# Kernel tuning notes

Hardware: AMD Instinct MI355X
Metric: run time of the kernel (lower is better)

Reference implementation:

```python
import jax, jax.numpy as jnp
import numpy as np
from jax import lax

K = 8  # diffusion channels
T = 3  # diffusion steps


def setup_inputs() -> dict:
    key = jax.random.key(0)
    k1, k2, k3 = jax.random.split(key, 3)
    x = jax.random.normal(k1, (16, 1, 512, 512), dtype=jnp.float32)
    # per-step conv weights [T, out=k, in=1, kh, kw] and biases [T, k]
    W = jax.random.normal(k2, (T, K, 1, 3, 3), dtype=jnp.float32) * 0.1
    b = jax.random.normal(k3, (T, K), dtype=jnp.float32) * 0.1
    return {"x": x, "W": W, "b": b}


def _g(d):
    # mode 1 edge-stopping function: exp(-|d| / (1 + d^2))
    return jnp.exp(-jnp.abs(d) / (1.0 + d * d))


def reference(x, W, b):
    in_x = x  # [N,1,H,W]
    for t in range(T):
        d1 = lax.conv_general_dilated(
            in_x, W[t], window_strides=(1, 1), padding="SAME",
            dimension_numbers=("NCHW", "OIHW", "NCHW"),
        ) + b[t][None, :, None, None]  # [N,K,H,W]
        features = _g(d1) * d1
        # squash_tensor: sum over the K channels, keep channel dim of 1
        in_x = in_x - jnp.sum(features, axis=1, keepdims=True) / K
    return in_x
```

## Files before the change

### kernel.cpp

```cpp
#include <hip/hip_runtime.h>

static constexpr int IMG = 512;
static constexpr int TX  = 64;
static constexpr int TY  = 16;
static constexpr int LST = 72;
static constexpr int SROWS  = TY + 6;
static constexpr int NSTAGE = SROWS * 18;

template<int WOFF, int NR, int RLO, int NG, bool TO_GLOBAL>
__device__ __forceinline__ void diffuse_step(
    const float* __restrict__ prev, float* __restrict__ cur,
    const float* __restrict__ Wt, const float* __restrict__ bt,
    int xoff, int ty0, int tx0, int tid, float* __restrict__ gout)
{
    constexpr int LOADW  = WOFF ? 8 : 6;
    constexpr int NITEMS = NR * NG;

    float L0[LOADW], L1[LOADW], L2[LOADW];
    {
        const int idx0 = (tid < NITEMS) ? tid : 0;
        const int rr = idx0 / NG, j = idx0 - rr * NG;
        const float* base = prev + (RLO + rr - 1) * LST + 4 * j;
        *(float4*)&L0[0] = *(const float4*)(base);
        *(float4*)&L1[0] = *(const float4*)(base + LST);
        *(float4*)&L2[0] = *(const float4*)(base + 2 * LST);
        if (WOFF) {
            *(float4*)&L0[4] = *(const float4*)(base + 4);
            *(float4*)&L1[4] = *(const float4*)(base + LST + 4);
            *(float4*)&L2[4] = *(const float4*)(base + 2 * LST + 4);
        } else {
            *(float2*)&L0[4] = *(const float2*)(base + 4);
            *(float2*)&L1[4] = *(const float2*)(base + LST + 4);
            *(float2*)&L2[4] = *(const float2*)(base + 2 * LST + 4);
        }
    }

    for (int idx = tid; idx < NITEMS; idx += 64) {
        float P0[LOADW], P1[LOADW], P2[LOADW];
        {
            const int nidx = (idx + 64 < NITEMS) ? (idx + 64) : idx;
            const int rr = nidx / NG, j = nidx - rr * NG;
            const float* base = prev + (RLO + rr - 1) * LST + 4 * j;
            *(float4*)&P0[0] = *(const float4*)(base);
            *(float4*)&P1[0] = *(const float4*)(base + LST);
            *(float4*)&P2[0] = *(const float4*)(base + 2 * LST);
            if (WOFF) {
                *(float4*)&P0[4] = *(const float4*)(base + 4);
                *(float4*)&P1[4] = *(const float4*)(base + LST + 4);
                *(float4*)&P2[4] = *(const float4*)(base + 2 * LST + 4);
            } else {
                *(float2*)&P0[4] = *(const float2*)(base + 4);
                *(float2*)&P1[4] = *(const float2*)(base + LST + 4);
                *(float2*)&P2[4] = *(const float2*)(base + 2 * LST + 4);
            }
        }

        const int rr = idx / NG, j = idx - rr * NG;
        const int r  = RLO + rr, c0 = 4 * j;

        float acc[4] = {0.f, 0.f, 0.f, 0.f};
#pragma unroll
        for (int k = 0; k < 8; ++k) {
            const float w0 = Wt[9*k+0], w1 = Wt[9*k+1], w2 = Wt[9*k+2];
            const float w3 = Wt[9*k+3], w4 = Wt[9*k+4], w5 = Wt[9*k+5];
            const float w6 = Wt[9*k+6], w7 = Wt[9*k+7], w8 = Wt[9*k+8];
            const float bk = bt[k];
#pragma unroll
            for (int i = 0; i < 4; ++i) {
                float d = bk;
                d = fmaf(w0, L0[WOFF+i],   d);
                d = fmaf(w1, L0[WOFF+i+1], d);
                d = fmaf(w2, L0[WOFF+i+2], d);
                d = fmaf(w3, L1[WOFF+i],   d);
                d = fmaf(w4, L1[WOFF+i+1], d);
                d = fmaf(w5, L1[WOFF+i+2], d);
                d = fmaf(w6, L2[WOFF+i],   d);
                d = fmaf(w7, L2[WOFF+i+1], d);
                d = fmaf(w8, L2[WOFF+i+2], d);
                const float t    = fmaf(d, d, 1.0f);
                const float rinv = __builtin_amdgcn_rcpf(t);
                const float e    = __builtin_amdgcn_exp2f(
                                       -1.442695040888963f * __builtin_fabsf(d) * rinv);
                acc[i] = fmaf(e, d, acc[i]);
            }
        }

        float4 v;
        v.x = L1[WOFF+1] - acc[0] * 0.125f;
        v.y = L1[WOFF+2] - acc[1] * 0.125f;
        v.z = L1[WOFF+3] - acc[2] * 0.125f;
        v.w = L1[WOFF+4] - acc[3] * 0.125f;

        const int gy = ty0 - 3 + r;
        if (TO_GLOBAL) {
            *(float4*)&gout[gy * IMG + tx0 + c0] = v;
        } else {
            const bool ry  = (unsigned)gy < (unsigned)IMG;
            const int  gx0 = xoff + c0;
            v.x = (ry && (unsigned)(gx0 + 0) < (unsigned)IMG) ? v.x : 0.f;
            v.y = (ry && (unsigned)(gx0 + 1) < (unsigned)IMG) ? v.y : 0.f;
            v.z = (ry && (unsigned)(gx0 + 2) < (unsigned)IMG) ? v.z : 0.f;
            v.w = (ry && (unsigned)(gx0 + 3) < (unsigned)IMG) ? v.w : 0.f;
            *(float4*)&cur[r * LST + c0] = v;
        }

#pragma unroll
        for (int q = 0; q < LOADW; ++q) { L0[q] = P0[q]; L1[q] = P1[q]; L2[q] = P2[q]; }
    }
}

__global__ __launch_bounds__(64) void deep_ad_kernel(
    const float* __restrict__ x, const float* __restrict__ W,
    const float* __restrict__ b, float* __restrict__ out)
{
    __shared__ float A[SROWS * LST];
    __shared__ float Bs[SROWS * LST];

    const int tid = threadIdx.x;
    const int tx0 = blockIdx.x * TX;
    const int ty0 = blockIdx.y * TY;
    const float* xin  = x   + (size_t)blockIdx.z * (IMG * IMG);
    float*       gout = out + (size_t)blockIdx.z * (IMG * IMG);

    {
        float4 sv[7];
#pragma unroll
        for (int q = 0; q < 7; ++q) {
            const int item = tid + 64 * q;
            const int rr = item / 18, j = item - rr * 18;
            const int gy = ty0 - 3 + rr;
            const int gx = tx0 - 4 + 4 * j;
            float4 v = {0.f, 0.f, 0.f, 0.f};
            if (item < NSTAGE && (unsigned)gy < (unsigned)IMG && (unsigned)gx < (unsigned)IMG)
                v = *(const float4*)(xin + gy * IMG + gx);
            sv[q] = v;
        }
#pragma unroll
        for (int q = 0; q < 7; ++q) {
            const int item = tid + 64 * q;
            if (item < NSTAGE) *(float4*)&A[item * 4] = sv[q];
        }
    }
    __syncthreads();

    diffuse_step<1, TY + 4, 1, 17, false>(A,  Bs, W + 0,   b + 0,  tx0 - 2, ty0, tx0, tid, nullptr);
    __syncthreads();
    diffuse_step<0, TY + 2, 2, 17, false>(Bs, A,  W + 72,  b + 8,  tx0 - 1, ty0, tx0, tid, nullptr);
    __syncthreads();
    diffuse_step<0, TY,     3, 16, true >(A, nullptr, W + 144, b + 16, 0, ty0, tx0, tid, gout);
}

extern "C" void kernel_launch(void* const* d_in, const int* in_sizes, int n_in,
                              void* d_out, int out_size, void* d_ws, size_t ws_size,
                              hipStream_t stream)
{
    const float* x = (const float*)d_in[0];
    const float* W = (const float*)d_in[1];
    const float* b = (const float*)d_in[2];
    float* out = (float*)d_out;
    const int N = in_sizes[0] / (IMG * IMG);
    dim3 grid(IMG / TX, IMG / TY, N);
    deep_ad_kernel<<<grid, 64, 0, stream>>>(x, W, b, out);
}
```

Measured before the change: 126.7 us.

## Double tile height and block size, fully unroll per-thread work loop

Tile height goes from 16 to 32 rows and the block from 64 to 128 threads. This cuts the fraction of halo rows recomputed across the three fused diffusion steps (recompute overhead drops from about 10/16 toward 10/32 of rows). The work loop becomes a compile-time unrolled trip count with clamped indices and guarded stores, so the last trip runs partially idle. Shared memory per block roughly doubles and the grid has half as many blocks, which may reduce occupancy and tail balance.

```diff
diff --git a/kernel.cpp b/kernel.cpp
--- a/kernel.cpp
+++ b/kernel.cpp
@@ -2,7 +2,8 @@
 
 static constexpr int IMG = 512;
 static constexpr int TX  = 64;
-static constexpr int TY  = 16;
+static constexpr int TY  = 32;
+static constexpr int NT  = 128;
 static constexpr int LST = 72;
 static constexpr int SROWS  = TY + 6;
 static constexpr int NSTAGE = SROWS * 18;
@@ -15,11 +16,12 @@
 {
     constexpr int LOADW  = WOFF ? 8 : 6;
     constexpr int NITEMS = NR * NG;
+    constexpr int TRIPS  = (NITEMS + NT - 1) / NT;
 
     float L0[LOADW], L1[LOADW], L2[LOADW];
     {
-        const int idx0 = (tid < NITEMS) ? tid : 0;
-        const int rr = idx0 / NG, j = idx0 - rr * NG;
+        const int cidx = (tid < NITEMS) ? tid : (NITEMS - 1);
+        const int rr = cidx / NG, j = cidx - rr * NG;
         const float* base = prev + (RLO + rr - 1) * LST + 4 * j;
         *(float4*)&L0[0] = *(const float4*)(base);
         *(float4*)&L1[0] = *(const float4*)(base + LST);
@@ -35,10 +37,14 @@
         }
     }
 
-    for (int idx = tid; idx < NITEMS; idx += 64) {
+#pragma unroll
+    for (int q = 0; q < TRIPS; ++q) {
+        const int idx = tid + q * NT;
+
         float P0[LOADW], P1[LOADW], P2[LOADW];
-        {
-            const int nidx = (idx + 64 < NITEMS) ? (idx + 64) : idx;
+        if (q + 1 < TRIPS) {
+            const int nidx = (tid + (q + 1) * NT < NITEMS) ? (tid + (q + 1) * NT)
+                                                           : (NITEMS - 1);
             const int rr = nidx / NG, j = nidx - rr * NG;
             const float* base = prev + (RLO + rr - 1) * LST + 4 * j;
             *(float4*)&P0[0] = *(const float4*)(base);
@@ -55,7 +61,8 @@
             }
         }
 
-        const int rr = idx / NG, j = idx - rr * NG;
+        const int cidx = (idx < NITEMS) ? idx : (NITEMS - 1);
+        const int rr = cidx / NG, j = cidx - rr * NG;
         const int r  = RLO + rr, c0 = 4 * j;
 
         float acc[4] = {0.f, 0.f, 0.f, 0.f};
@@ -93,7 +100,8 @@
 
         const int gy = ty0 - 3 + r;
         if (TO_GLOBAL) {
-            *(float4*)&gout[gy * IMG + tx0 + c0] = v;
+            if (idx < NITEMS)
+                *(float4*)&gout[gy * IMG + tx0 + c0] = v;
         } else {
             const bool ry  = (unsigned)gy < (unsigned)IMG;
             const int  gx0 = xoff + c0;
@@ -101,15 +109,16 @@
             v.y = (ry && (unsigned)(gx0 + 1) < (unsigned)IMG) ? v.y : 0.f;
             v.z = (ry && (unsigned)(gx0 + 2) < (unsigned)IMG) ? v.z : 0.f;
             v.w = (ry && (unsigned)(gx0 + 3) < (unsigned)IMG) ? v.w : 0.f;
-            *(float4*)&cur[r * LST + c0] = v;
+            if (idx < NITEMS)
+                *(float4*)&cur[r * LST + c0] = v;
         }
 
 #pragma unroll
-        for (int q = 0; q < LOADW; ++q) { L0[q] = P0[q]; L1[q] = P1[q]; L2[q] = P2[q]; }
+        for (int qq = 0; qq < LOADW; ++qq) { L0[qq] = P0[qq]; L1[qq] = P1[qq]; L2[qq] = P2[qq]; }
     }
 }
 
-__global__ __launch_bounds__(64) void deep_ad_kernel(
+__global__ __launch_bounds__(NT) void deep_ad_kernel(
     const float* __restrict__ x, const float* __restrict__ W,
     const float* __restrict__ b, float* __restrict__ out)
 {
@@ -123,10 +132,11 @@
     float*       gout = out + (size_t)blockIdx.z * (IMG * IMG);
 
     {
-        float4 sv[7];
+        constexpr int SQ = (NSTAGE + NT - 1) / NT;
+        float4 sv[SQ];
 #pragma unroll
-        for (int q = 0; q < 7; ++q) {
-            const int item = tid + 64 * q;
+        for (int q = 0; q < SQ; ++q) {
+            const int item = tid + NT * q;
             const int rr = item / 18, j = item - rr * 18;
             const int gy = ty0 - 3 + rr;
             const int gx = tx0 - 4 + 4 * j;
@@ -136,8 +146,8 @@
             sv[q] = v;
         }
 #pragma unroll
-        for (int q = 0; q < 7; ++q) {
-            const int item = tid + 64 * q;
+        for (int q = 0; q < SQ; ++q) {
+            const int item = tid + NT * q;
             if (item < NSTAGE) *(float4*)&A[item * 4] = sv[q];
         }
     }
@@ -160,5 +170,5 @@
     float* out = (float*)d_out;
     const int N = in_sizes[0] / (IMG * IMG);
     dim3 grid(IMG / TX, IMG / TY, N);
-    deep_ad_kernel<<<grid, 64, 0, stream>>>(x, W, b, out);
+    deep_ad_kernel<<<grid, NT, 0, stream>>>(x, W, b, out);
 }
```

Result: no change. 125.6 us (-0.9%).

## Split fused three-step diffusion into per-step kernels via workspace

Applied to the files above, without the earlier changes.

Adds a standalone per-step kernel with 256-thread blocks that reads neighbors directly from global memory. When the workspace is large enough, it runs three launches ping-ponging between the output and workspace instead of the fused shared-memory kernel. This removes halo recomputation and the low-occupancy 64-thread blocks, but adds global round trips of intermediate images and extra launches.

```diff
diff --git a/kernel.cpp b/kernel.cpp
--- a/kernel.cpp
+++ b/kernel.cpp
@@ -1,10 +1,80 @@
 #include <hip/hip_runtime.h>
 
 static constexpr int IMG = 512;
-static constexpr int TX  = 64;
-static constexpr int TY  = 16;
+
+__device__ __forceinline__ float gd_acc(float d, float acc) {
+    const float t    = fmaf(d, d, 1.0f);
+    const float rinv = __builtin_amdgcn_rcpf(t);
+    const float e    = __builtin_amdgcn_exp2f(
+                           -1.442695040888963f * __builtin_fabsf(d) * rinv);
+    return fmaf(e, d, acc);
+}
+
+__global__ __launch_bounds__(256) void ad_step(
+    const float* __restrict__ in, float* __restrict__ outp,
+    const float* __restrict__ Wt, const float* __restrict__ bt)
+{
+    const int tid = threadIdx.x;
+    const int x0  = blockIdx.x * 64 + (tid & 15) * 4;
+    const int y   = blockIdx.y * 16 + (tid >> 4);
+    const float* __restrict__ src = in + (size_t)blockIdx.z * (IMG * IMG);
+
+    float L[3][12];
+    const bool xfast = (x0 >= 4) && (x0 <= 504);
+#pragma unroll
+    for (int dy = 0; dy < 3; ++dy) {
+        const int yy = y + dy - 1;
+        const bool rowok = (unsigned)yy < (unsigned)IMG;
+        if (xfast && rowok) {
+            const float* p = src + yy * IMG + x0 - 4;
+            *(float4*)&L[dy][0] = *(const float4*)(p);
+            *(float4*)&L[dy][4] = *(const float4*)(p + 4);
+            *(float4*)&L[dy][8] = *(const float4*)(p + 8);
+        } else {
+#pragma unroll
+            for (int j = 0; j < 12; ++j) {
+                const int col = x0 - 4 + j;
+                L[dy][j] = (rowok && (unsigned)col < (unsigned)IMG)
+                               ? src[yy * IMG + col] : 0.f;
+            }
+        }
+    }
+
+    float acc[4] = {0.f, 0.f, 0.f, 0.f};
+#pragma unroll
+    for (int k = 0; k < 8; ++k) {
+        const float w0 = Wt[9*k+0], w1 = Wt[9*k+1], w2 = Wt[9*k+2];
+        const float w3 = Wt[9*k+3], w4 = Wt[9*k+4], w5 = Wt[9*k+5];
+        const float w6 = Wt[9*k+6], w7 = Wt[9*k+7], w8 = Wt[9*k+8];
+        const float bk = bt[k];
+#pragma unroll
+        for (int i = 0; i < 4; ++i) {
+            float d = bk;
+            d = fmaf(w0, L[0][i+3], d);
+            d = fmaf(w1, L[0][i+4], d);
+            d = fmaf(w2, L[0][i+5], d);
+            d = fmaf(w3, L[1][i+3], d);
+            d = fmaf(w4, L[1][i+4], d);
+            d = fmaf(w5, L[1][i+5], d);
+            d = fmaf(w6, L[2][i+3], d);
+            d = fmaf(w7, L[2][i+4], d);
+            d = fmaf(w8, L[2][i+5], d);
+            acc[i] = gd_acc(d, acc[i]);
+        }
+    }
+
+    float4 v;
+    v.x = L[1][4] - acc[0] * 0.125f;
+    v.y = L[1][5] - acc[1] * 0.125f;
+    v.z = L[1][6] - acc[2] * 0.125f;
+    v.w = L[1][7] - acc[3] * 0.125f;
+    *(float4*)&outp[(size_t)blockIdx.z * (IMG * IMG) + y * IMG + x0] = v;
+}
+
+static constexpr int TXF = 64;
+static constexpr int TYF = 16;
 static constexpr int LST = 72;
-static constexpr int SROWS  = TY + 6;
+static constexpr int SROWS  = TYF + 6;
 static constexpr int NSTAGE = SROWS * 18;
 
 template<int WOFF, int NR, int RLO, int NG, bool TO_GLOBAL>
@@ -77,11 +147,7 @@
                 d = fmaf(w6, L2[WOFF+i],   d);
                 d = fmaf(w7, L2[WOFF+i+1], d);
                 d = fmaf(w8, L2[WOFF+i+2], d);
-                const float t    = fmaf(d, d, 1.0f);
-                const float rinv = __builtin_amdgcn_rcpf(t);
-                const float e    = __builtin_amdgcn_exp2f(
-                                       -1.442695040888963f * __builtin_fabsf(d) * rinv);
-                acc[i] = fmaf(e, d, acc[i]);
+                acc[i] = gd_acc(d, acc[i]);
             }
         }
 
@@ -109,7 +175,7 @@
     }
 }
 
-__global__ __launch_bounds__(64) void deep_ad_kernel(
+__global__ __launch_bounds__(64) void deep_ad_fused(
     const float* __restrict__ x, const float* __restrict__ W,
     const float* __restrict__ b, float* __restrict__ out)
 {
@@ -117,8 +183,8 @@
     __shared__ float Bs[SROWS * LST];
 
     const int tid = threadIdx.x;
-    const int tx0 = blockIdx.x * TX;
-    const int ty0 = blockIdx.y * TY;
+    const int tx0 = blockIdx.x * TXF;
+    const int ty0 = blockIdx.y * TYF;
     const float* xin  = x   + (size_t)blockIdx.z * (IMG * IMG);
     float*       gout = out + (size_t)blockIdx.z * (IMG * IMG);
 
@@ -143,11 +209,11 @@
     }
     __syncthreads();
 
-    diffuse_step<1, TY + 4, 1, 17, false>(A,  Bs, W + 0,   b + 0,  tx0 - 2, ty0, tx0, tid, nullptr);
+    diffuse_step<1, TYF + 4, 1, 17, false>(A,  Bs, W + 0,   b + 0,  tx0 - 2, ty0, tx0, tid, nullptr);
     __syncthreads();
-    diffuse_step<0, TY + 2, 2, 17, false>(Bs, A,  W + 72,  b + 8,  tx0 - 1, ty0, tx0, tid, nullptr);
+    diffuse_step<0, TYF + 2, 2, 17, false>(Bs, A,  W + 72,  b + 8,  tx0 - 1, ty0, tx0, tid, nullptr);
     __syncthreads();
-    diffuse_step<0, TY,     3, 16, true >(A, nullptr, W + 144, b + 16, 0, ty0, tx0, tid, gout);
+    diffuse_step<0, TYF,     3, 16, true >(A, nullptr, W + 144, b + 16, 0, ty0, tx0, tid, gout);
 }
 
 extern "C" void kernel_launch(void* const* d_in, const int* in_sizes, int n_in,
@@ -159,6 +225,16 @@
     const float* b = (const float*)d_in[2];
     float* out = (float*)d_out;
     const int N = in_sizes[0] / (IMG * IMG);
-    dim3 grid(IMG / TX, IMG / TY, N);
-    deep_ad_kernel<<<grid, 64, 0, stream>>>(x, W, b, out);
-}
+
+    const size_t imgBytes = (size_t)N * IMG * IMG * sizeof(float);
+    if (ws_size >= imgBytes) {
+        float* ws = (float*)d_ws;
+        dim3 g(IMG / 64, IMG / 16, N);
+        ad_step<<<g, 256, 0, stream>>>(x,   out, W + 0,   b + 0);
+        ad_step<<<g, 256, 0, stream>>>(out, ws,  W + 72,  b + 8);
+        ad_step<<<g, 256, 0, stream>>>(ws,  out, W + 144, b + 16);
+    } else {
+        dim3 grid(IMG / TXF, IMG / TYF, N);
+        deep_ad_fused<<<grid, 64, 0, stream>>>(x, W, b, out);
+    }
+}
```

New measurement: 115.3 us. -9.1%, faster.
